# Performance work log

Measured on AMD Instinct MI355X. Metric: run time of the kernel, lower is better.

## Reference

```python
import jax, jax.numpy as jnp
import numpy as np

N = 50000
IN_F = 512
HID = 64
HEADS = 4
CLASSES = 6
E = 800000
NEG_SLOPE = 0.2


def setup_inputs() -> dict:
    key = jax.random.key(0)
    ks = jax.random.split(key, 12)
    s = 1.0 / np.sqrt(IN_F)
    s2 = 1.0 / np.sqrt(HID * HEADS)
    return {
        "x": jax.random.normal(ks[0], (N, IN_F), dtype=jnp.float32),
        "edge_index": jax.random.randint(ks[1], (2, E), 0, N, dtype=jnp.int32),
        "W1": jax.random.normal(ks[2], (IN_F, HEADS * HID), dtype=jnp.float32) * s,
        "a_src1": jax.random.normal(ks[3], (HEADS, HID), dtype=jnp.float32) * s,
        "a_dst1": jax.random.normal(ks[4], (HEADS, HID), dtype=jnp.float32) * s,
        "b1": jnp.zeros((HEADS * HID,), dtype=jnp.float32),
        "W2": jax.random.normal(ks[5], (HEADS * HID, CLASSES), dtype=jnp.float32) * s2,
        "a_src2": jax.random.normal(ks[6], (1, CLASSES), dtype=jnp.float32) * s2,
        "a_dst2": jax.random.normal(ks[7], (1, CLASSES), dtype=jnp.float32) * s2,
        "b2": jnp.zeros((CLASSES,), dtype=jnp.float32),
    }


def gat_conv(x, src, dst, W, a_src, a_dst, bias, heads, ch):
    # x: [N, F] -> h: [N, H, C]
    n = x.shape[0]
    h = (x @ W).reshape(n, heads, ch)
    # per-node attention halves: [N, H]
    e_src = jnp.einsum('nhc,hc->nh', h, a_src)
    e_dst = jnp.einsum('nhc,hc->nh', h, a_dst)
    # per-edge logits with leaky relu: [E', H]
    logits = jax.nn.leaky_relu(e_src[src] + e_dst[dst], NEG_SLOPE)
    # segment softmax over incoming edges of each dst node
    m = jax.ops.segment_max(logits, dst, num_segments=n)  # [N, H]
    p = jnp.exp(logits - m[dst])
    denom = jax.ops.segment_sum(p, dst, num_segments=n)   # [N, H] (>0: self loops)
    alpha = p / denom[dst]                                 # [E', H]
    # weighted scatter-aggregate: [N, H, C]
    out = jax.ops.segment_sum(alpha[:, :, None] * h[src], dst, num_segments=n)
    return out.reshape(n, heads * ch) + bias


def reference(x, edge_index, W1, a_src1, a_dst1, b1, W2, a_src2, a_dst2, b2):
    n = x.shape[0]
    loops = jnp.arange(n, dtype=edge_index.dtype)
    src = jnp.concatenate([edge_index[0], loops])  # PyG add_self_loops
    dst = jnp.concatenate([edge_index[1], loops])
    h = gat_conv(x, src, dst, W1, a_src1, a_dst1, b1, HEADS, HID)
    h = jax.nn.elu(h)
    out = gat_conv(h, src, dst, W2, a_src2, a_dst2, b2, 1, CLASSES)
    return jax.nn.log_softmax(out, axis=1)
```

## Files before the change

### kernel.cpp

```cpp
#include <hip/hip_runtime.h>

#define HEADS 4
#define HID 64
#define CH1 256
#define CLS 6
#define NSLOPE 0.2f

typedef short bf16x8 __attribute__((ext_vector_type(8)));
typedef float f32x4 __attribute__((ext_vector_type(4)));

__device__ __forceinline__ float leaky(float x) {
  return (x >= 0.f) ? x : NSLOPE * x;
}

__device__ __forceinline__ ushort f2bf(float f) {
  unsigned u = __float_as_uint(f);
  unsigned r = (u + 0x7FFFu + ((u >> 16) & 1u)) >> 16;
  return (ushort)r;
}

__device__ __forceinline__ float bf2f(ushort u) {
  return __uint_as_float((unsigned)u << 16);
}

__device__ __forceinline__ void gload16(const void* g, void* l) {
  __builtin_amdgcn_global_load_lds((const __attribute__((address_space(1))) void*)g,
                                   (__attribute__((address_space(3))) void*)l, 16, 0, 0);
}

__global__ void k_cvt(const float* __restrict__ in, ushort* __restrict__ out, long n) {
  long i = ((long)blockIdx.x * 256 + threadIdx.x) * 4;
  long stride = (long)gridDim.x * 1024;
  for (; i + 3 < n; i += stride) {
    float4 v = *(const float4*)&in[i];
    ushort4 o;
    o.x = f2bf(v.x); o.y = f2bf(v.y); o.z = f2bf(v.z); o.w = f2bf(v.w);
    *(ushort4*)&out[i] = o;
  }
}

__global__ void k_cvt_w1t(const float* __restrict__ W1, ushort* __restrict__ w1t) {
  int t = blockIdx.x * 256 + threadIdx.x;
  if (t >= 512 * 256) return;
  int k = t >> 8, c = t & 255;
  w1t[c * 512 + k] = f2bf(W1[t]);
}

__global__ __launch_bounds__(256) void k_gemm1_mfma(
    const ushort* __restrict__ xb,
    const ushort* __restrict__ w1t,
    const float* __restrict__ a_src, const float* __restrict__ a_dst,
    ushort* __restrict__ h1b, float* __restrict__ es, float* __restrict__ ed,
    int M) {
  __shared__ ushort lds[2][10240];
  int t = threadIdx.x;
  int wid = t >> 6, lane = t & 63;
  int brow = blockIdx.x * 64;

  int rA = t >> 2;
  int sA = (t & 3) ^ (rA & 3);
  int rowA = brow + rA; if (rowA >= M) rowA = M - 1;
  const ushort* srcA  = xb  + (size_t)rowA * 512 + sA * 8;
  int cB = t >> 2;
  int sB = (t & 3) ^ (cB & 3);
  const ushort* srcB0 = w1t + (size_t)cB * 512 + sB * 8;
  int dA = t * 8;
  int dB = 2048 + t * 8;

  int l15 = lane & 15, g = lane >> 4;
  int sw = ((g ^ (lane & 3)) << 3);
  int aoff[4], boff[4];
#pragma unroll
  for (int m = 0; m < 4; ++m) aoff[m] = (m * 16 + l15) * 32 + sw;
#pragma unroll
  for (int n = 0; n < 4; ++n) boff[n] = 2048 + (wid * 64 + n * 16 + l15) * 32 + sw;

  f32x4 acc[4][4] = {};

#define STAGE(buf, koff) do { \
    gload16(srcA + (koff),              &lds[buf][dA]); \
    gload16(srcB0 + (koff),             &lds[buf][dB]); \
    gload16(srcB0 +  64 * 512 + (koff), &lds[buf][dB + 2048]); \
    gload16(srcB0 + 128 * 512 + (koff), &lds[buf][dB + 4096]); \
    gload16(srcB0 + 192 * 512 + (koff), &lds[buf][dB + 6144]); \
  } while (0)

  STAGE(0, 0);
  __syncthreads();
  int cur = 0;
  for (int kt = 0; kt < 16; ++kt) {
    if (kt < 15) STAGE(cur ^ 1, (kt + 1) * 32);
    const ushort* L = lds[cur];
    bf16x8 av[4], bv[4];
#pragma unroll
    for (int m = 0; m < 4; ++m) av[m] = *(const bf16x8*)&L[aoff[m]];
#pragma unroll
    for (int n = 0; n < 4; ++n) bv[n] = *(const bf16x8*)&L[boff[n]];
#pragma unroll
    for (int m = 0; m < 4; ++m)
#pragma unroll
      for (int n = 0; n < 4; ++n)
        acc[m][n] = __builtin_amdgcn_mfma_f32_16x16x32_bf16(av[m], bv[n], acc[m][n], 0, 0, 0);
    __syncthreads();
    cur ^= 1;
  }
#undef STAGE

  float as4[4], ad4[4];
#pragma unroll
  for (int n = 0; n < 4; ++n) {
    int c = wid * 64 + n * 16 + l15;
    as4[n] = a_src[c];
    ad4[n] = a_dst[c];
  }
  int rbase = g * 4;
#pragma unroll
  for (int m = 0; m < 4; ++m) {
#pragma unroll
    for (int r = 0; r < 4; ++r) {
      int grow = brow + m * 16 + rbase + r;
      bool ok = grow < M;
      float ps = 0.f, pd = 0.f;
#pragma unroll
      for (int n = 0; n < 4; ++n) {
        float v = acc[m][n][r];
        ps += v * as4[n];
        pd += v * ad4[n];
        if (ok) h1b[(size_t)grow * CH1 + wid * 64 + n * 16 + l15] = f2bf(v);
      }
#pragma unroll
      for (int o = 1; o < 16; o <<= 1) {
        ps += __shfl_xor(ps, o);
        pd += __shfl_xor(pd, o);
      }
      if (l15 == 0 && ok) {
        es[grow * HEADS + wid] = ps;
        ed[grow * HEADS + wid] = pd;
      }
    }
  }
}

__global__ void k_count(const int* __restrict__ ei, int E, int Etot,
                        int* __restrict__ cnt) {
  int e = blockIdx.x * blockDim.x + threadIdx.x;
  if (e >= Etot) return;
  int d = (e < E) ? ei[E + e] : e - E;
  atomicAdd(&cnt[d], 1);
}

__global__ __launch_bounds__(256) void k_scan1(const int* __restrict__ deg,
    int* __restrict__ rowptr, int* __restrict__ bsum, int n) {
  int i = blockIdx.x * 256 + threadIdx.x;
  int v = (i < n) ? deg[i] : 0;
  int lane = threadIdx.x & 63, wave = threadIdx.x >> 6;
  int incl = v;
#pragma unroll
  for (int o = 1; o < 64; o <<= 1) {
    int u = __shfl_up(incl, o);
    if (lane >= o) incl += u;
  }
  __shared__ int ws4[4];
  if (lane == 63) ws4[wave] = incl;
  __syncthreads();
  if (threadIdx.x == 0) {
    int run = 0;
    for (int w = 0; w < 4; ++w) { int x = ws4[w]; ws4[w] = run; run += x; }
    bsum[blockIdx.x] = run;
  }
  __syncthreads();
  if (i < n) rowptr[i] = incl - v + ws4[wave];
}

__global__ __launch_bounds__(256) void k_scan2(int* __restrict__ bsum, int nb) {
  int t = threadIdx.x;
  int v = (t < nb) ? bsum[t] : 0;
  int lane = t & 63, wave = t >> 6;
  int incl = v;
#pragma unroll
  for (int o = 1; o < 64; o <<= 1) {
    int u = __shfl_up(incl, o);
    if (lane >= o) incl += u;
  }
  __shared__ int ws4[4];
  if (lane == 63) ws4[wave] = incl;
  __syncthreads();
  if (t == 0) {
    int run = 0;
    for (int w = 0; w < 4; ++w) { int x = ws4[w]; ws4[w] = run; run += x; }
  }
  __syncthreads();
  if (t < nb) bsum[t] = incl - v + ws4[wave];
}

__global__ void k_scan3(int* __restrict__ rowptr, const int* __restrict__ bsum,
                        int n, int Etot) {
  int i = blockIdx.x * 256 + threadIdx.x;
  if (i < n) rowptr[i] += bsum[blockIdx.x];
  if (i == 0) rowptr[n] = Etot;
}

__global__ void k_scatter(const int* __restrict__ ei, int E, int Etot,
    const int* __restrict__ rowptr, int* __restrict__ cursor,
    int* __restrict__ esrc) {
  int e = blockIdx.x * blockDim.x + threadIdx.x;
  if (e >= Etot) return;
  int s, d;
  if (e < E) { s = ei[e]; d = ei[E + e]; } else { s = d = e - E; }
  int pos = rowptr[d] + atomicAdd(&cursor[d], 1);
  esrc[pos] = s;
}

__global__ __launch_bounds__(256) void k_agg1_csr(const int* __restrict__ rowptr,
    const int* __restrict__ esrc, const float* __restrict__ es,
    const float* __restrict__ ed, const ushort* __restrict__ h1b,
    const float* __restrict__ b1, float* __restrict__ out1, int Nn) {
  __shared__ int   spi[4][64];
  __shared__ float spp[4][64 * 4];
  int wid = threadIdx.x >> 6, lane = threadIdx.x & 63;
  int d = blockIdx.x * 4 + wid;
  if (d >= Nn) return;
  int beg = rowptr[d], end = rowptr[d + 1];
  float4 edv = *(const float4*)&ed[d * 4];
  int myhead = lane >> 4;
  int ch = lane * 4;

  float4 m4 = make_float4(-1e30f, -1e30f, -1e30f, -1e30f);
  for (int i = beg + lane; i < end; i += 64) {
    int s = esrc[i];
    float4 e4 = *(const float4*)&es[s * 4];
    m4.x = fmaxf(m4.x, leaky(e4.x + edv.x));
    m4.y = fmaxf(m4.y, leaky(e4.y + edv.y));
    m4.z = fmaxf(m4.z, leaky(e4.z + edv.z));
    m4.w = fmaxf(m4.w, leaky(e4.w + edv.w));
  }
#pragma unroll
  for (int o = 32; o; o >>= 1) {
    m4.x = fmaxf(m4.x, __shfl_xor(m4.x, o));
    m4.y = fmaxf(m4.y, __shfl_xor(m4.y, o));
    m4.z = fmaxf(m4.z, __shfl_xor(m4.z, o));
    m4.w = fmaxf(m4.w, __shfl_xor(m4.w, o));
  }

  float4 acc = make_float4(0.f, 0.f, 0.f, 0.f);
  float4 den4 = make_float4(0.f, 0.f, 0.f, 0.f);
  const float* pp = &spp[wid][0];
  for (int c0 = beg; c0 < end; c0 += 64) {
    int i = c0 + lane;
    int s = 0;
    float4 p = make_float4(0.f, 0.f, 0.f, 0.f);
    if (i < end) {
      s = esrc[i];
      float4 e4 = *(const float4*)&es[s * 4];
      p.x = __expf(leaky(e4.x + edv.x) - m4.x);
      p.y = __expf(leaky(e4.y + edv.y) - m4.y);
      p.z = __expf(leaky(e4.z + edv.z) - m4.z);
      p.w = __expf(leaky(e4.w + edv.w) - m4.w);
    }
    den4.x += p.x; den4.y += p.y; den4.z += p.z; den4.w += p.w;
    spi[wid][lane] = s;
    *(float4*)&spp[wid][lane * 4] = p;
    int cl = min(64, end - c0);
    int j = 0;
    for (; j + 3 < cl; j += 4) {
      int s0 = spi[wid][j],     s1 = spi[wid][j + 1];
      int s2 = spi[wid][j + 2], s3 = spi[wid][j + 3];
      float p0 = pp[j * 4 + myhead],       p1 = pp[(j + 1) * 4 + myhead];
      float p2 = pp[(j + 2) * 4 + myhead], p3 = pp[(j + 3) * 4 + myhead];
      ushort4 v0 = *(const ushort4*)&h1b[(size_t)s0 * CH1 + ch];
      ushort4 v1 = *(const ushort4*)&h1b[(size_t)s1 * CH1 + ch];
      ushort4 v2 = *(const ushort4*)&h1b[(size_t)s2 * CH1 + ch];
      ushort4 v3 = *(const ushort4*)&h1b[(size_t)s3 * CH1 + ch];
      acc.x += p0 * bf2f(v0.x) + p1 * bf2f(v1.x) + p2 * bf2f(v2.x) + p3 * bf2f(v3.x);
      acc.y += p0 * bf2f(v0.y) + p1 * bf2f(v1.y) + p2 * bf2f(v2.y) + p3 * bf2f(v3.y);
      acc.z += p0 * bf2f(v0.z) + p1 * bf2f(v1.z) + p2 * bf2f(v2.z) + p3 * bf2f(v3.z);
      acc.w += p0 * bf2f(v0.w) + p1 * bf2f(v1.w) + p2 * bf2f(v2.w) + p3 * bf2f(v3.w);
    }
    for (; j < cl; ++j) {
      int sj = spi[wid][j];
      float pj = pp[j * 4 + myhead];
      ushort4 v = *(const ushort4*)&h1b[(size_t)sj * CH1 + ch];
      acc.x += pj * bf2f(v.x);
      acc.y += pj * bf2f(v.y);
      acc.z += pj * bf2f(v.z);
      acc.w += pj * bf2f(v.w);
    }
  }
#pragma unroll
  for (int o = 32; o; o >>= 1) {
    den4.x += __shfl_xor(den4.x, o);
    den4.y += __shfl_xor(den4.y, o);
    den4.z += __shfl_xor(den4.z, o);
    den4.w += __shfl_xor(den4.w, o);
  }
  float den = (myhead == 0) ? den4.x : (myhead == 1) ? den4.y
            : (myhead == 2) ? den4.z : den4.w;
  float4 b4 = *(const float4*)&b1[ch];
  float4 r;
  r.x = acc.x / den + b4.x; r.x = (r.x > 0.f) ? r.x : expm1f(r.x);
  r.y = acc.y / den + b4.y; r.y = (r.y > 0.f) ? r.y : expm1f(r.y);
  r.z = acc.z / den + b4.z; r.z = (r.z > 0.f) ? r.z : expm1f(r.z);
  r.w = acc.w / den + b4.w; r.w = (r.w > 0.f) ? r.w : expm1f(r.w);
  *(float4*)&out1[(size_t)d * CH1 + ch] = r;
}

__global__ __launch_bounds__(256) void k_gemm2(const float* __restrict__ h,
    const float* __restrict__ W2, const float* __restrict__ a_src2,
    const float* __restrict__ a_dst2, float* __restrict__ h2,
    float* __restrict__ es2, float* __restrict__ ed2, int Nn) {
  __shared__ float w[CH1][CLS];
  for (int i = threadIdx.x; i < CH1 * CLS; i += 256)
    w[i / CLS][i % CLS] = W2[i];
  __syncthreads();
  int n = blockIdx.x * 256 + threadIdx.x;
  if (n >= Nn) return;
  const float* hr = &h[(size_t)n * CH1];
  float a0 = 0.f, a1 = 0.f, a2 = 0.f, a3 = 0.f, a4 = 0.f, a5 = 0.f;
#pragma unroll 8
  for (int k = 0; k < CH1; k += 4) {
    float4 x = *(const float4*)&hr[k];
    a0 += x.x * w[k][0] + x.y * w[k + 1][0] + x.z * w[k + 2][0] + x.w * w[k + 3][0];
    a1 += x.x * w[k][1] + x.y * w[k + 1][1] + x.z * w[k + 2][1] + x.w * w[k + 3][1];
    a2 += x.x * w[k][2] + x.y * w[k + 1][2] + x.z * w[k + 2][2] + x.w * w[k + 3][2];
    a3 += x.x * w[k][3] + x.y * w[k + 1][3] + x.z * w[k + 2][3] + x.w * w[k + 3][3];
    a4 += x.x * w[k][4] + x.y * w[k + 1][4] + x.z * w[k + 2][4] + x.w * w[k + 3][4];
    a5 += x.x * w[k][5] + x.y * w[k + 1][5] + x.z * w[k + 2][5] + x.w * w[k + 3][5];
  }
  float* h2r = &h2[(size_t)n * CLS];
  h2r[0] = a0; h2r[1] = a1; h2r[2] = a2; h2r[3] = a3; h2r[4] = a4; h2r[5] = a5;
  es2[n] = a0 * a_src2[0] + a1 * a_src2[1] + a2 * a_src2[2]
         + a3 * a_src2[3] + a4 * a_src2[4] + a5 * a_src2[5];
  ed2[n] = a0 * a_dst2[0] + a1 * a_dst2[1] + a2 * a_dst2[2]
         + a3 * a_dst2[3] + a4 * a_dst2[4] + a5 * a_dst2[5];
}

__global__ __launch_bounds__(256) void k_l2(const int* __restrict__ rowptr,
    const int* __restrict__ esrc, const float* __restrict__ es2,
    const float* __restrict__ ed2, const float* __restrict__ h2,
    const float* __restrict__ b2, float* __restrict__ out, int Nn) {
  int w = (blockIdx.x * 256 + threadIdx.x) >> 6;
  int lane = threadIdx.x & 63;
  if (w >= Nn) return;
  int beg = rowptr[w], end = rowptr[w + 1];
  float edv = ed2[w];
  float m = -1e30f;
  for (int i = beg + lane; i < end; i += 64)
    m = fmaxf(m, leaky(es2[esrc[i]] + edv));
#pragma unroll
  for (int o = 32; o; o >>= 1) m = fmaxf(m, __shfl_xor(m, o));
  float den = 0.f, a0 = 0.f, a1 = 0.f, a2 = 0.f, a3 = 0.f, a4 = 0.f, a5 = 0.f;
  for (int i = beg + lane; i < end; i += 64) {
    int s = esrc[i];
    float p = __expf(leaky(es2[s] + edv) - m);
    den += p;
    const float* hr = &h2[s * CLS];
    a0 += p * hr[0]; a1 += p * hr[1]; a2 += p * hr[2];
    a3 += p * hr[3]; a4 += p * hr[4]; a5 += p * hr[5];
  }
#pragma unroll
  for (int o = 32; o; o >>= 1) {
    den += __shfl_xor(den, o);
    a0 += __shfl_xor(a0, o); a1 += __shfl_xor(a1, o); a2 += __shfl_xor(a2, o);
    a3 += __shfl_xor(a3, o); a4 += __shfl_xor(a4, o); a5 += __shfl_xor(a5, o);
  }
  if (lane == 0) {
    float v[CLS];
    v[0] = a0 / den + b2[0]; v[1] = a1 / den + b2[1]; v[2] = a2 / den + b2[2];
    v[3] = a3 / den + b2[3]; v[4] = a4 / den + b2[4]; v[5] = a5 / den + b2[5];
    float mx = -1e30f;
#pragma unroll
    for (int j = 0; j < CLS; ++j) mx = fmaxf(mx, v[j]);
    float sum = 0.f;
#pragma unroll
    for (int j = 0; j < CLS; ++j) sum += __expf(v[j] - mx);
    float l = mx + logf(sum);
#pragma unroll
    for (int j = 0; j < CLS; ++j) out[w * CLS + j] = v[j] - l;
  }
}

extern "C" void kernel_launch(void* const* d_in, const int* in_sizes, int n_in,
                              void* d_out, int out_size, void* d_ws, size_t ws_size,
                              hipStream_t stream) {
  const float* x      = (const float*)d_in[0];
  const int*   ei     = (const int*)d_in[1];
  const float* W1     = (const float*)d_in[2];
  const float* a_src1 = (const float*)d_in[3];
  const float* a_dst1 = (const float*)d_in[4];
  const float* b1     = (const float*)d_in[5];
  const float* W2     = (const float*)d_in[6];
  const float* a_src2 = (const float*)d_in[7];
  const float* a_dst2 = (const float*)d_in[8];
  const float* b2     = (const float*)d_in[9];
  float* out = (float*)d_out;

  const int IN_F = 512;
  int N = in_sizes[0] / IN_F;
  int E = in_sizes[1] / 2;
  int Etot = E + N;

  float* ws = (float*)d_ws;
  size_t off = 0;
  ushort* h1b = (ushort*)(ws + off); off += (size_t)N * CH1;
  float* out1 = ws + off; off += (size_t)N * CH1;
  float* es1  = ws + off; off += (size_t)N * HEADS;
  float* ed1  = ws + off; off += (size_t)N * HEADS;
  float* h2   = ws + off; off += (size_t)N * CLS;
  float* es2  = ws + off; off += (size_t)N;
  float* ed2  = ws + off; off += (size_t)N;
  int* rowptr = (int*)(ws + off); off += (size_t)N + 1;
  int* cursor = (int*)(ws + off); off += (size_t)N;
  int* bsum   = (int*)(ws + off); off += 256;
  int* esrc   = (int*)(ws + off); off += (size_t)Etot;
  ushort* w1t = (ushort*)(ws + off); off += (512 * 256 * 2 + 3) / 4;
  ushort* xb  = (ushort*)out1;

  int nb = (N + 255) / 256;
  int eb = (Etot + 255) / 256;

  hipMemsetAsync(cursor, 0, (size_t)N * 4, stream);
  k_count<<<eb, 256, 0, stream>>>(ei, E, Etot, cursor);
  k_scan1<<<nb, 256, 0, stream>>>(cursor, rowptr, bsum, N);
  k_scan2<<<1, 256, 0, stream>>>(bsum, nb);
  k_scan3<<<nb, 256, 0, stream>>>(rowptr, bsum, N, Etot);
  hipMemsetAsync(cursor, 0, (size_t)N * 4, stream);
  k_scatter<<<eb, 256, 0, stream>>>(ei, E, Etot, rowptr, cursor, esrc);

  k_cvt<<<2048, 256, 0, stream>>>(x, xb, (long)N * IN_F);
  k_cvt_w1t<<<(512 * 256 + 255) / 256, 256, 0, stream>>>(W1, w1t);
  k_gemm1_mfma<<<(N + 63) / 64, 256, 0, stream>>>(xb, w1t, a_src1, a_dst1,
                                                  h1b, es1, ed1, N);
  k_agg1_csr<<<(N + 3) / 4, 256, 0, stream>>>(rowptr, esrc, es1, ed1, h1b, b1, out1, N);

  k_gemm2<<<(N + 255) / 256, 256, 0, stream>>>(out1, W2, a_src2, a_dst2,
                                               h2, es2, ed2, N);
  k_l2<<<(N * 64 + 255) / 256, 256, 0, stream>>>(rowptr, esrc, es2, ed2, h2, b2, out, N);
}
```

Baseline: 293.4 us.

## Fuse x fp32-to-bf16 conversion into GEMM1, regroup layer-2 aggregation per 8 lanes

Drops the separate x conversion kernel. GEMM1 now streams fp32 x tiles into LDS with a swizzled layout and packs them to bf16 with v_cvt_pk_bf16_f32 before the MFMAs, which removes a full write and re-read of the 50000x512 bf16 copy. Layer-2 aggregation now gives each node 8 lanes instead of a 64-lane wave, which suits the ~17 average in-degree, and pads h2 rows to 8 floats so they load as float4/float2. Layer-1 aggregation precomputes byte offsets to save address math. In exchange the GEMM1 A tile doubles in LDS footprint and adds conversion ALU work inside the K loop.

```diff
diff --git a/kernel.cpp b/kernel.cpp
--- a/kernel.cpp
+++ b/kernel.cpp
@@ -4,6 +4,7 @@
 #define HID 64
 #define CH1 256
 #define CLS 6
+#define H2S 8
 #define NSLOPE 0.2f
 
 typedef short bf16x8 __attribute__((ext_vector_type(8)));
@@ -26,17 +27,6 @@
 __device__ __forceinline__ void gload16(const void* g, void* l) {
   __builtin_amdgcn_global_load_lds((const __attribute__((address_space(1))) void*)g,
                                    (__attribute__((address_space(3))) void*)l, 16, 0, 0);
-}
-
-__global__ void k_cvt(const float* __restrict__ in, ushort* __restrict__ out, long n) {
-  long i = ((long)blockIdx.x * 256 + threadIdx.x) * 4;
-  long stride = (long)gridDim.x * 1024;
-  for (; i + 3 < n; i += stride) {
-    float4 v = *(const float4*)&in[i];
-    ushort4 o;
-    o.x = f2bf(v.x); o.y = f2bf(v.y); o.z = f2bf(v.z); o.w = f2bf(v.w);
-    *(ushort4*)&out[i] = o;
-  }
 }
 
 __global__ void k_cvt_w1t(const float* __restrict__ W1, ushort* __restrict__ w1t) {
@@ -47,55 +37,72 @@
 }
 
 __global__ __launch_bounds__(256) void k_gemm1_mfma(
-    const ushort* __restrict__ xb,
+    const float* __restrict__ x,
     const ushort* __restrict__ w1t,
     const float* __restrict__ a_src, const float* __restrict__ a_dst,
     ushort* __restrict__ h1b, float* __restrict__ es, float* __restrict__ ed,
     int M) {
-  __shared__ ushort lds[2][10240];
+  __shared__ float  ldsA[2][2048];
+  __shared__ ushort ldsB[2][8192];
   int t = threadIdx.x;
   int wid = t >> 6, lane = t & 63;
   int brow = blockIdx.x * 64;
 
-  int rA = t >> 2;
-  int sA = (t & 3) ^ (rA & 3);
-  int rowA = brow + rA; if (rowA >= M) rowA = M - 1;
-  const ushort* srcA  = xb  + (size_t)rowA * 512 + sA * 8;
+  int rA0 = t >> 3,         ls0 = (t & 7) ^ (rA0 & 7);
+  int rA1 = (t + 256) >> 3, ls1 = ((t + 256) & 7) ^ (rA1 & 7);
+  int rowA0 = brow + rA0; if (rowA0 >= M) rowA0 = M - 1;
+  int rowA1 = brow + rA1; if (rowA1 >= M) rowA1 = M - 1;
+  const float* srcA0 = x + (size_t)rowA0 * 512 + ls0 * 4;
+  const float* srcA1 = x + (size_t)rowA1 * 512 + ls1 * 4;
+  int dA = t * 4;
+
   int cB = t >> 2;
   int sB = (t & 3) ^ (cB & 3);
   const ushort* srcB0 = w1t + (size_t)cB * 512 + sB * 8;
-  int dA = t * 8;
-  int dB = 2048 + t * 8;
+  int dB = t * 8;
 
   int l15 = lane & 15, g = lane >> 4;
-  int sw = ((g ^ (lane & 3)) << 3);
-  int aoff[4], boff[4];
-#pragma unroll
-  for (int m = 0; m < 4; ++m) aoff[m] = (m * 16 + l15) * 32 + sw;
-#pragma unroll
-  for (int n = 0; n < 4; ++n) boff[n] = 2048 + (wid * 64 + n * 16 + l15) * 32 + sw;
+  int swb = ((g ^ (lane & 3)) << 3);
+  int aoff0[4], aoff1[4], boff[4];
+#pragma unroll
+  for (int m = 0; m < 4; ++m) {
+    int r = m * 16 + l15;
+    aoff0[m] = r * 32 + ((2 * g) ^ (r & 7)) * 4;
+    aoff1[m] = r * 32 + ((2 * g + 1) ^ (r & 7)) * 4;
+  }
+#pragma unroll
+  for (int n = 0; n < 4; ++n) boff[n] = (wid * 64 + n * 16 + l15) * 32 + swb;
 
   f32x4 acc[4][4] = {};
 
-#define STAGE(buf, koff) do { \
-    gload16(srcA + (koff),              &lds[buf][dA]); \
-    gload16(srcB0 + (koff),             &lds[buf][dB]); \
-    gload16(srcB0 +  64 * 512 + (koff), &lds[buf][dB + 2048]); \
-    gload16(srcB0 + 128 * 512 + (koff), &lds[buf][dB + 4096]); \
-    gload16(srcB0 + 192 * 512 + (koff), &lds[buf][dB + 6144]); \
+#define STAGE(buf, kt) do { \
+    gload16(srcA0 + (kt) * 32,            &ldsA[buf][dA]); \
+    gload16(srcA1 + (kt) * 32,            &ldsA[buf][1024 + dA]); \
+    gload16(srcB0 + (kt) * 32,            &ldsB[buf][dB]); \
+    gload16(srcB0 +  64 * 512 + (kt) * 32, &ldsB[buf][dB + 2048]); \
+    gload16(srcB0 + 128 * 512 + (kt) * 32, &ldsB[buf][dB + 4096]); \
+    gload16(srcB0 + 192 * 512 + (kt) * 32, &ldsB[buf][dB + 6144]); \
   } while (0)
 
   STAGE(0, 0);
   __syncthreads();
   int cur = 0;
   for (int kt = 0; kt < 16; ++kt) {
-    if (kt < 15) STAGE(cur ^ 1, (kt + 1) * 32);
-    const ushort* L = lds[cur];
+    if (kt < 15) STAGE(cur ^ 1, kt + 1);
     bf16x8 av[4], bv[4];
 #pragma unroll
-    for (int m = 0; m < 4; ++m) av[m] = *(const bf16x8*)&L[aoff[m]];
-#pragma unroll
-    for (int n = 0; n < 4; ++n) bv[n] = *(const bf16x8*)&L[boff[n]];
+    for (int m = 0; m < 4; ++m) {
+      f32x4 lo = *(const f32x4*)&ldsA[cur][aoff0[m]];
+      f32x4 hi = *(const f32x4*)&ldsA[cur][aoff1[m]];
+      union { unsigned u[4]; bf16x8 b; } cv;
+      asm("v_cvt_pk_bf16_f32 %0, %1, %2" : "=v"(cv.u[0]) : "v"(lo[0]), "v"(lo[1]));
+      asm("v_cvt_pk_bf16_f32 %0, %1, %2" : "=v"(cv.u[1]) : "v"(lo[2]), "v"(lo[3]));
+      asm("v_cvt_pk_bf16_f32 %0, %1, %2" : "=v"(cv.u[2]) : "v"(hi[0]), "v"(hi[1]));
+      asm("v_cvt_pk_bf16_f32 %0, %1, %2" : "=v"(cv.u[3]) : "v"(hi[2]), "v"(hi[3]));
+      av[m] = cv.b;
+    }
+#pragma unroll
+    for (int n = 0; n < 4; ++n) bv[n] = *(const bf16x8*)&ldsB[cur][boff[n]];
 #pragma unroll
     for (int m = 0; m < 4; ++m)
 #pragma unroll
@@ -224,6 +231,7 @@
   float4 edv = *(const float4*)&ed[d * 4];
   int myhead = lane >> 4;
   int ch = lane * 4;
+  const char* hcb = (const char*)h1b + (size_t)ch * 2;
 
   float4 m4 = make_float4(-1e30f, -1e30f, -1e30f, -1e30f);
   for (int i = beg + lane; i < end; i += 64) {
@@ -258,28 +266,28 @@
       p.w = __expf(leaky(e4.w + edv.w) - m4.w);
     }
     den4.x += p.x; den4.y += p.y; den4.z += p.z; den4.w += p.w;
-    spi[wid][lane] = s;
+    spi[wid][lane] = s << 9;
     *(float4*)&spp[wid][lane * 4] = p;
     int cl = min(64, end - c0);
     int j = 0;
     for (; j + 3 < cl; j += 4) {
-      int s0 = spi[wid][j],     s1 = spi[wid][j + 1];
-      int s2 = spi[wid][j + 2], s3 = spi[wid][j + 3];
+      int o0 = spi[wid][j],     o1 = spi[wid][j + 1];
+      int o2 = spi[wid][j + 2], o3 = spi[wid][j + 3];
       float p0 = pp[j * 4 + myhead],       p1 = pp[(j + 1) * 4 + myhead];
       float p2 = pp[(j + 2) * 4 + myhead], p3 = pp[(j + 3) * 4 + myhead];
-      ushort4 v0 = *(const ushort4*)&h1b[(size_t)s0 * CH1 + ch];
-      ushort4 v1 = *(const ushort4*)&h1b[(size_t)s1 * CH1 + ch];
-      ushort4 v2 = *(const ushort4*)&h1b[(size_t)s2 * CH1 + ch];
-      ushort4 v3 = *(const ushort4*)&h1b[(size_t)s3 * CH1 + ch];
+      ushort4 v0 = *(const ushort4*)(hcb + o0);
+      ushort4 v1 = *(const ushort4*)(hcb + o1);
+      ushort4 v2 = *(const ushort4*)(hcb + o2);
+      ushort4 v3 = *(const ushort4*)(hcb + o3);
       acc.x += p0 * bf2f(v0.x) + p1 * bf2f(v1.x) + p2 * bf2f(v2.x) + p3 * bf2f(v3.x);
       acc.y += p0 * bf2f(v0.y) + p1 * bf2f(v1.y) + p2 * bf2f(v2.y) + p3 * bf2f(v3.y);
       acc.z += p0 * bf2f(v0.z) + p1 * bf2f(v1.z) + p2 * bf2f(v2.z) + p3 * bf2f(v3.z);
       acc.w += p0 * bf2f(v0.w) + p1 * bf2f(v1.w) + p2 * bf2f(v2.w) + p3 * bf2f(v3.w);
     }
     for (; j < cl; ++j) {
-      int sj = spi[wid][j];
+      int oj = spi[wid][j];
       float pj = pp[j * 4 + myhead];
-      ushort4 v = *(const ushort4*)&h1b[(size_t)sj * CH1 + ch];
+      ushort4 v = *(const ushort4*)(hcb + oj);
       acc.x += pj * bf2f(v.x);
       acc.y += pj * bf2f(v.y);
       acc.z += pj * bf2f(v.z);
@@ -326,7 +334,7 @@
     a4 += x.x * w[k][4] + x.y * w[k + 1][4] + x.z * w[k + 2][4] + x.w * w[k + 3][4];
     a5 += x.x * w[k][5] + x.y * w[k + 1][5] + x.z * w[k + 2][5] + x.w * w[k + 3][5];
   }
-  float* h2r = &h2[(size_t)n * CLS];
+  float* h2r = &h2[(size_t)n * H2S];
   h2r[0] = a0; h2r[1] = a1; h2r[2] = a2; h2r[3] = a3; h2r[4] = a4; h2r[5] = a5;
   es2[n] = a0 * a_src2[0] + a1 * a_src2[1] + a2 * a_src2[2]
          + a3 * a_src2[3] + a4 * a_src2[4] + a5 * a_src2[5];
@@ -338,32 +346,36 @@
     const int* __restrict__ esrc, const float* __restrict__ es2,
     const float* __restrict__ ed2, const float* __restrict__ h2,
     const float* __restrict__ b2, float* __restrict__ out, int Nn) {
-  int w = (blockIdx.x * 256 + threadIdx.x) >> 6;
-  int lane = threadIdx.x & 63;
-  if (w >= Nn) return;
-  int beg = rowptr[w], end = rowptr[w + 1];
-  float edv = ed2[w];
+  int t = threadIdx.x;
+  int grp = t >> 3, sl = t & 7;
+  int n = blockIdx.x * 32 + grp;
+  if (n >= Nn) return;
+  int beg = rowptr[n], end = rowptr[n + 1];
+  float edv = ed2[n];
   float m = -1e30f;
-  for (int i = beg + lane; i < end; i += 64)
+  for (int i = beg + sl; i < end; i += 8)
     m = fmaxf(m, leaky(es2[esrc[i]] + edv));
-#pragma unroll
-  for (int o = 32; o; o >>= 1) m = fmaxf(m, __shfl_xor(m, o));
+  m = fmaxf(m, __shfl_xor(m, 1));
+  m = fmaxf(m, __shfl_xor(m, 2));
+  m = fmaxf(m, __shfl_xor(m, 4));
   float den = 0.f, a0 = 0.f, a1 = 0.f, a2 = 0.f, a3 = 0.f, a4 = 0.f, a5 = 0.f;
-  for (int i = beg + lane; i < end; i += 64) {
+  for (int i = beg + sl; i < end; i += 8) {
     int s = esrc[i];
     float p = __expf(leaky(es2[s] + edv) - m);
     den += p;
-    const float* hr = &h2[s * CLS];
-    a0 += p * hr[0]; a1 += p * hr[1]; a2 += p * hr[2];
-    a3 += p * hr[3]; a4 += p * hr[4]; a5 += p * hr[5];
-  }
-#pragma unroll
-  for (int o = 32; o; o >>= 1) {
+    const float* hr = &h2[(size_t)s * H2S];
+    float4 v0 = *(const float4*)hr;
+    float2 v1 = *(const float2*)(hr + 4);
+    a0 += p * v0.x; a1 += p * v0.y; a2 += p * v0.z;
+    a3 += p * v0.w; a4 += p * v1.x; a5 += p * v1.y;
+  }
+#pragma unroll
+  for (int o = 1; o < 8; o <<= 1) {
     den += __shfl_xor(den, o);
     a0 += __shfl_xor(a0, o); a1 += __shfl_xor(a1, o); a2 += __shfl_xor(a2, o);
     a3 += __shfl_xor(a3, o); a4 += __shfl_xor(a4, o); a5 += __shfl_xor(a5, o);
   }
-  if (lane == 0) {
+  if (sl == 0) {
     float v[CLS];
     v[0] = a0 / den + b2[0]; v[1] = a1 / den + b2[1]; v[2] = a2 / den + b2[2];
     v[3] = a3 / den + b2[3]; v[4] = a4 / den + b2[4]; v[5] = a5 / den + b2[5];
@@ -375,7 +387,7 @@
     for (int j = 0; j < CLS; ++j) sum += __expf(v[j] - mx);
     float l = mx + logf(sum);
 #pragma unroll
-    for (int j = 0; j < CLS; ++j) out[w * CLS + j] = v[j] - l;
+    for (int j = 0; j < CLS; ++j) out[n * CLS + j] = v[j] - l;
   }
 }
 
@@ -405,7 +417,7 @@
   float* out1 = ws + off; off += (size_t)N * CH1;
   float* es1  = ws + off; off += (size_t)N * HEADS;
   float* ed1  = ws + off; off += (size_t)N * HEADS;
-  float* h2   = ws + off; off += (size_t)N * CLS;
+  float* h2   = ws + off; off += (size_t)N * H2S;
   float* es2  = ws + off; off += (size_t)N;
   float* ed2  = ws + off; off += (size_t)N;
   int* rowptr = (int*)(ws + off); off += (size_t)N + 1;
@@ -413,7 +425,6 @@
   int* bsum   = (int*)(ws + off); off += 256;
   int* esrc   = (int*)(ws + off); off += (size_t)Etot;
   ushort* w1t = (ushort*)(ws + off); off += (512 * 256 * 2 + 3) / 4;
-  ushort* xb  = (ushort*)out1;
 
   int nb = (N + 255) / 256;
   int eb = (Etot + 255) / 256;
@@ -426,13 +437,12 @@
   hipMemsetAsync(cursor, 0, (size_t)N * 4, stream);
   k_scatter<<<eb, 256, 0, stream>>>(ei, E, Etot, rowptr, cursor, esrc);
 
-  k_cvt<<<2048, 256, 0, stream>>>(x, xb, (long)N * IN_F);
   k_cvt_w1t<<<(512 * 256 + 255) / 256, 256, 0, stream>>>(W1, w1t);
-  k_gemm1_mfma<<<(N + 63) / 64, 256, 0, stream>>>(xb, w1t, a_src1, a_dst1,
+  k_gemm1_mfma<<<(N + 63) / 64, 256, 0, stream>>>(x, w1t, a_src1, a_dst1,
                                                   h1b, es1, ed1, N);
   k_agg1_csr<<<(N + 3) / 4, 256, 0, stream>>>(rowptr, esrc, es1, ed1, h1b, b1, out1, N);
 
   k_gemm2<<<(N + 255) / 256, 256, 0, stream>>>(out1, W2, a_src2, a_dst2,
                                                h2, es2, ed2, N);
-  k_l2<<<(N * 64 + 255) / 256, 256, 0, stream>>>(rowptr, esrc, es2, ed2, h2, b2, out, N);
-}
+  k_l2<<<(N + 31) / 32, 256, 0, stream>>>(rowptr, esrc, es2, ed2, h2, b2, out, N);
+}
```

Result: faster. 267.2 us (-8.9%).
